# Kernel tuning notes

Hardware: AMD Instinct MI355X
Metric: run time of the kernel (lower is better)

Reference implementation:

```python
import jax, jax.numpy as jnp
import numpy as np

RATIO = 0.25
RADIUS = 0.2
K = 32  # max_num_neighbors


def fps_single(pos, M):
    """Farthest point sampling on one cloud. pos: [N,3] -> idx [M] (start at index 0)."""
    d0 = jnp.sum((pos - pos[0]) ** 2, axis=-1)  # [N] min sq-dist to selected set

    def step(mind, _):
        nxt = jnp.argmax(mind)
        d = jnp.sum((pos - pos[nxt]) ** 2, axis=-1)
        return jnp.minimum(mind, d), nxt

    _, rest = jax.lax.scan(step, d0, None, length=M - 1)
    return jnp.concatenate([jnp.zeros((1,), dtype=rest.dtype), rest])


def mlp(h, W0, b0, W1, b1, W2, b2):
    h = jax.nn.relu(h @ W0 + b0)
    h = jax.nn.relu(h @ W1 + b1)
    h = jax.nn.relu(h @ W2 + b2)
    return h


def setup_inputs() -> dict:
    key = jax.random.key(0)
    ks = jax.random.split(key, 8)
    B, N, C = 8, 8192, 64
    x = jax.random.normal(ks[0], (B, N, C), dtype=jnp.float32)
    pos = jax.random.uniform(ks[1], (B, N, 3), dtype=jnp.float32)
    W0 = jax.random.normal(ks[2], (C + 3, 64), dtype=jnp.float32) * 0.05
    b0 = jnp.zeros((64,), dtype=jnp.float32)
    W1 = jax.random.normal(ks[3], (64, 64), dtype=jnp.float32) * 0.05
    b1 = jnp.zeros((64,), dtype=jnp.float32)
    W2 = jax.random.normal(ks[4], (64, 128), dtype=jnp.float32) * 0.05
    b2 = jnp.zeros((128,), dtype=jnp.float32)
    return {"x": x, "pos": pos, "W0": W0, "b0": b0, "W1": W1, "b1": b1, "W2": W2, "b2": b2}


def reference(x, pos, W0, b0, W1, b1, W2, b2):
    B, N, C = x.shape
    M = int(N * RATIO)
    # 1) FPS per cloud
    idx = jax.vmap(lambda p: fps_single(p, M))(pos)                 # [B, M]
    pos_s = jnp.take_along_axis(pos, idx[..., None], axis=1)        # [B, M, 3]
    # 2) radius ball query: k-nearest (k=K) then mask out > radius.
    #    neighbor selection carries no gradient in the original -> stop_gradient.
    d2 = jax.lax.stop_gradient(
        jnp.sum((pos_s[:, :, None, :] - pos[:, None, :, :]) ** 2, axis=-1))  # [B, M, N]
    negd, nbr = jax.lax.top_k(-d2, K)                               # [B, M, K]
    valid = (-negd) <= RADIUS ** 2                                  # self is always valid (d=0)
    # 3) gather + PointConv message: mlp(concat(x_j, pos_j - pos_i)), max aggr
    x_j = jax.vmap(lambda xb, ib: xb[ib])(x, nbr)                   # [B, M, K, C]
    pos_j = jax.vmap(lambda pb, ib: pb[ib])(pos, nbr)               # [B, M, K, 3]
    feat = jnp.concatenate([x_j, pos_j - pos_s[:, :, None, :]], axis=-1)  # [B, M, K, C+3]
    h = mlp(feat, W0, b0, W1, b1, W2, b2)                           # [B, M, K, 128]
    h = jnp.where(valid[..., None], h, jnp.full_like(h, -1e9))
    x1 = jnp.max(h, axis=2)                                         # [B, M, 128]
    return x1, pos_s
```

## Files before the change

kernel.cpp:

```cpp
#include <hip/hip_runtime.h>
#include <hip/hip_bf16.h>
#include <hip/hip_fp16.h>

#define NB 8
#define NP 8192
#define NC 64
#define NM 2048
#define NK 32
#define RAD2 0.04f

typedef unsigned int u32;
typedef unsigned long long u64;
typedef _Float16 f16x8 __attribute__((ext_vector_type(8)));
typedef float f32x4 __attribute__((ext_vector_type(4)));

__device__ __forceinline__ float d2e(float ax, float ay, float az,
                                     float bx, float by, float bz) {
    float dx = __fsub_rn(ax, bx), dy = __fsub_rn(ay, by), dz = __fsub_rn(az, bz);
    return __fadd_rn(__fadd_rn(__fmul_rn(dx, dx), __fmul_rn(dy, dy)), __fmul_rn(dz, dz));
}

__device__ __forceinline__ int spread3(int v) {
    return (v & 1) | ((v & 2) << 2) | ((v & 4) << 4);
}

#define RED64(CTRL) do {                                                              \
    u32 hi_ = (u32)(k >> 32), lo_ = (u32)k;                                           \
    u32 h2_ = (u32)__builtin_amdgcn_update_dpp((int)hi_, (int)hi_, (CTRL), 0xF, 0xF, false); \
    u32 l2_ = (u32)__builtin_amdgcn_update_dpp((int)lo_, (int)lo_, (CTRL), 0xF, 0xF, false); \
    u64 o_ = ((u64)h2_ << 32) | l2_;                                                  \
    if (o_ > k) k = o_;                                                               \
} while (0)

#define DPPF(V, CTRL) __int_as_float(__builtin_amdgcn_update_dpp(                     \
    __float_as_int(V), __float_as_int(V), (CTRL), 0xF, 0xF, false))

#define WREDMIN(V) do { V = fminf(V, DPPF(V, 0x111)); V = fminf(V, DPPF(V, 0x112));   \
    V = fminf(V, DPPF(V, 0x114)); V = fminf(V, DPPF(V, 0x118));                       \
    V = fminf(V, DPPF(V, 0x142)); V = fminf(V, DPPF(V, 0x143)); } while (0)
#define WREDMAX(V) do { V = fmaxf(V, DPPF(V, 0x111)); V = fmaxf(V, DPPF(V, 0x112));   \
    V = fmaxf(V, DPPF(V, 0x114)); V = fmaxf(V, DPPF(V, 0x118));                       \
    V = fmaxf(V, DPPF(V, 0x142)); V = fmaxf(V, DPPF(V, 0x143)); } while (0)

__device__ __forceinline__ float rl63(float v) {
    return __int_as_float(__builtin_amdgcn_readlane(__float_as_int(v), 63));
}

#define FPT 8
__global__ __launch_bounds__(1024, 1) void fps_kernel(const float* __restrict__ pos,
                                                      float* __restrict__ pos_s) {
    __shared__ float4 sp4[NP];
    __shared__ u32 hist[512], cursor[512];
    __shared__ u64 gkey[3];
    __shared__ u32 pos0srt;

    const int b = blockIdx.x;
    const int tid = threadIdx.x;
    const int lane = tid & 63;
    const float* pb = pos + (size_t)b * (NP * 3);

    float ax[FPT], ay[FPT], az[FPT];
    int key[FPT];
    {
        float f[24];
        const float4* src = (const float4*)(pb + tid * 24);
#pragma unroll
        for (int v = 0; v < 6; ++v) *(float4*)&f[v * 4] = src[v];
#pragma unroll
        for (int j = 0; j < FPT; ++j) {
            ax[j] = f[3 * j]; ay[j] = f[3 * j + 1]; az[j] = f[3 * j + 2];
            int qx = min(7, max(0, (int)(ax[j] * 8.0f)));
            int qy = min(7, max(0, (int)(ay[j] * 8.0f)));
            int qz = min(7, max(0, (int)(az[j] * 8.0f)));
            key[j] = (spread3(qx) << 2) | (spread3(qy) << 1) | spread3(qz);
        }
    }
    if (tid < 512) hist[tid] = 0;
    __syncthreads();
#pragma unroll
    for (int j = 0; j < FPT; ++j) atomicAdd(&hist[key[j]], 1);
    __syncthreads();
    for (int off = 1; off < 512; off <<= 1) {
        u32 v = 0;
        if (tid < 512 && tid >= off) v = hist[tid - off];
        __syncthreads();
        if (tid < 512) hist[tid] += v;
        __syncthreads();
    }
    if (tid < 512) cursor[tid] = (tid == 0) ? 0u : hist[tid - 1];
    if (tid == 0) { gkey[0] = 0; gkey[1] = 0; gkey[2] = 0; }
    __syncthreads();
#pragma unroll
    for (int j = 0; j < FPT; ++j) {
        int dst = (int)atomicAdd(&cursor[key[j]], 1);
        u32 orig = tid * FPT + j;
        sp4[dst] = make_float4(ax[j], ay[j], az[j],
                               __uint_as_float((8191u - orig) << 13));
        if (orig == 0) pos0srt = (u32)dst;
    }
    __syncthreads();

    const int base = tid * FPT;
    const float4 s0 = sp4[pos0srt];
    float px[FPT], py[FPT], pz[FPT];
    u64 mkey[FPT];
    float lox, hix, loy, hiy, loz, hiz;
#pragma unroll
    for (int j = 0; j < FPT; ++j) {
        float4 v = sp4[base + j];
        px[j] = v.x; py[j] = v.y; pz[j] = v.z;
        float d = d2e(v.x, v.y, v.z, s0.x, s0.y, s0.z);
        u32 lo = __float_as_uint(v.w) | (u32)(base + j);
        mkey[j] = ((u64)__float_as_uint(d) << 32) | lo;
        if (j == 0) {
            lox = hix = px[0]; loy = hiy = py[0]; loz = hiz = pz[0];
        } else {
            lox = fminf(lox, px[j]); hix = fmaxf(hix, px[j]);
            loy = fminf(loy, py[j]); hiy = fmaxf(hiy, py[j]);
            loz = fminf(loz, pz[j]); hiz = fmaxf(hiz, pz[j]);
        }
    }
    float wlox, whix, wloy, whiy, wloz, whiz;
    { float v;
      v = lox; WREDMIN(v); wlox = rl63(v);
      v = hix; WREDMAX(v); whix = rl63(v);
      v = loy; WREDMIN(v); wloy = rl63(v);
      v = hiy; WREDMAX(v); whiy = rl63(v);
      v = loz; WREDMIN(v); wloz = rl63(v);
      v = hiz; WREDMAX(v); whiz = rl63(v);
    }
    float* outp = pos_s + (size_t)b * (NM * 3);
    if (tid == 0) { outp[0] = s0.x; outp[1] = s0.y; outp[2] = s0.z; }
    u64 ck = mkey[0];
#pragma unroll
    for (int j = 1; j < FPT; ++j) ck = (mkey[j] > ck) ? mkey[j] : ck;
    u64 wkey;
    { u64 k = ck;
      RED64(0x111); RED64(0x112); RED64(0x114);
      RED64(0x118); RED64(0x142); RED64(0x143);
      wkey = k; }
    float wmindf = __uint_as_float((u32)(wkey >> 32));

    int slot = 1, prv = 0;
    for (int t = 1; t < NM; ++t) {
        if (lane == 63) atomicMax(&gkey[slot], wkey);
        __syncthreads();
        u64 gk = gkey[slot];
        if (tid == 0) gkey[prv] = 0;
        const int srt = (int)(gk & 0x1FFFu);
        const float4 sv = sp4[srt];
        if (tid == 0) { outp[3 * t] = sv.x; outp[3 * t + 1] = sv.y; outp[3 * t + 2] = sv.z; }
        float wgx = fmaxf(fmaxf(__fsub_rn(wlox, sv.x), __fsub_rn(sv.x, whix)), 0.0f);
        float wgy = fmaxf(fmaxf(__fsub_rn(wloy, sv.y), __fsub_rn(sv.y, whiy)), 0.0f);
        float wgz = fmaxf(fmaxf(__fsub_rn(wloz, sv.z), __fsub_rn(sv.z, whiz)), 0.0f);
        float wbnd = wgx * wgx + wgy * wgy + wgz * wgz;
        if (wbnd * 0.999999f < wmindf) {
            float gx = fmaxf(fmaxf(__fsub_rn(lox, sv.x), __fsub_rn(sv.x, hix)), 0.0f);
            float gy = fmaxf(fmaxf(__fsub_rn(loy, sv.y), __fsub_rn(sv.y, hiy)), 0.0f);
            float gz = fmaxf(fmaxf(__fsub_rn(loz, sv.z), __fsub_rn(sv.z, hiz)), 0.0f);
            float bnd = gx * gx + gy * gy + gz * gz;
            float cvf = __uint_as_float((u32)(ck >> 32));
            bool u = (bnd * 0.999999f < cvf);
            if (__ballot(u)) {
                __builtin_amdgcn_s_setprio(1);
                if (u) {
                    u64 nk = 0;
#pragma unroll
                    for (int j = 0; j < FPT; ++j) {
                        float d = d2e(px[j], py[j], pz[j], sv.x, sv.y, sv.z);
                        u32 hi = min((u32)(mkey[j] >> 32), __float_as_uint(d));
                        u64 nm = ((u64)hi << 32) | (u32)mkey[j];
                        mkey[j] = nm;
                        nk = (j == 0) ? nm : ((nm > nk) ? nm : nk);
                    }
                    ck = nk;
                }
                u64 k = ck;
                RED64(0x111); RED64(0x112); RED64(0x114);
                RED64(0x118); RED64(0x142); RED64(0x143);
                wkey = k;
                wmindf = __uint_as_float((u32)(wkey >> 32));
                __builtin_amdgcn_s_setprio(0);
            }
        }
        prv = slot; slot = (slot == 2) ? 0 : slot + 1;
    }
}

#define GQ 8
#define CAP 768
__global__ __launch_bounds__(256, 1) void knn_kernel(const float* __restrict__ pos,
                                                     const float* __restrict__ pos_s,
                                                     int* __restrict__ nbr) {
    __shared__ u64 keys[GQ][CAP];
    __shared__ int cnt[GQ];
    const int qbase = blockIdx.x * GQ;
    const int b = qbase >> 11;
    const int tid = threadIdx.x;
    if (tid < GQ) cnt[tid] = 0;
    for (int i = tid; i < GQ * NK; i += 256) nbr[qbase * NK + i] = -1;

    float qx[GQ], qy[GQ], qz[GQ];
#pragma unroll
    for (int q = 0; q < GQ; ++q) {
        qx[q] = pos_s[(qbase + q) * 3];
        qy[q] = pos_s[(qbase + q) * 3 + 1];
        qz[q] = pos_s[(qbase + q) * 3 + 2];
    }
    __syncthreads();

    const float* pb = pos + (size_t)b * (NP * 3);
    for (int i = 0; i < NP / 256; ++i) {
        int p = tid + (i << 8);
        float x = pb[3 * p], y = pb[3 * p + 1], z = pb[3 * p + 2];
#pragma unroll
        for (int q = 0; q < GQ; ++q) {
            float d = d2e(x, y, z, qx[q], qy[q], qz[q]);
            if (d <= RAD2) {
                int slot = atomicAdd(&cnt[q], 1);
                if (slot < CAP) keys[q][slot] = ((u64)__float_as_uint(d) << 32) | (u32)p;
            }
        }
    }
    __syncthreads();

    for (int q = 0; q < GQ; ++q) {
        int c = min(cnt[q], CAP);
        for (int j = tid; j < c; j += 256) {
            u64 key = keys[q][j];
            int rank = 0;
            for (int t2 = 0; t2 < c; ++t2) rank += (keys[q][t2] < key) ? 1 : 0;
            if (rank < NK) nbr[(qbase + q) * NK + rank] = (int)(u32)(key & 0xFFFFFFFFull);
        }
    }
}

#define FPAD 104
#define HPAD 72
#define TG 8
__global__ __launch_bounds__(512, 1) void mlp_kernel(
    const float* __restrict__ x, const float* __restrict__ pos,
    const float* __restrict__ W0, const float* __restrict__ b0,
    const float* __restrict__ W1, const float* __restrict__ b1,
    const float* __restrict__ W2, const float* __restrict__ b2,
    const float* __restrict__ pos_s, const int* __restrict__ nbr,
    float* __restrict__ x1) {
    __shared__ _Float16 feat[256 * FPAD];
    __shared__ _Float16 h1[256 * HPAD];
    __shared__ _Float16 wt0[64 * FPAD];
    __shared__ _Float16 wt1[64 * HPAD];
    __shared__ _Float16 wt2[128 * HPAD];
    __shared__ float bias0[64], bias1[64], bias2[128];
    __shared__ int vld[256];

    const int tid = threadIdx.x;
    const int g0 = blockIdx.x * TG;
    const int b = g0 >> 11;

    for (int idx = tid; idx < 64 * FPAD; idx += 512) {
        int c2 = idx / FPAD, j = idx - c2 * FPAD;
        wt0[idx] = (_Float16)((j < 67) ? W0[j * 64 + c2] : 0.0f);
    }
    for (int idx = tid; idx < 64 * HPAD; idx += 512) {
        int c2 = idx / HPAD, j = idx - c2 * HPAD;
        wt1[idx] = (_Float16)((j < 64) ? W1[j * 64 + c2] : 0.0f);
    }
    for (int idx = tid; idx < 128 * HPAD; idx += 512) {
        int c2 = idx / HPAD, j = idx - c2 * HPAD;
        wt2[idx] = (_Float16)((j < 64) ? W2[j * 128 + c2] : 0.0f);
    }
    if (tid < 64) { bias0[tid] = b0[tid]; bias1[tid] = b1[tid]; }
    else if (tid < 192) bias2[tid - 64] = b2[tid - 64];

    {
        int r = tid >> 1, half = tid & 1;
        int g = g0 + (r >> 5), k = r & 31;
        int nid = nbr[g * NK + k];
        int nid2 = nid < 0 ? 0 : nid;
        const float* xr = x + ((size_t)b * NP + nid2) * NC + half * 32;
        _Float16* dst = &feat[r * FPAD + half * 32];
#pragma unroll
        for (int i = 0; i < 8; ++i) {
            float4 v = *(const float4*)(xr + i * 4);
            dst[i * 4 + 0] = (_Float16)v.x; dst[i * 4 + 1] = (_Float16)v.y;
            dst[i * 4 + 2] = (_Float16)v.z; dst[i * 4 + 3] = (_Float16)v.w;
        }
        if (half) {
            const float* pj = pos + ((size_t)b * NP + nid2) * 3;
            const float* ps = pos_s + (size_t)g * 3;
            feat[r * FPAD + 64] = (_Float16)(pj[0] - ps[0]);
            feat[r * FPAD + 65] = (_Float16)(pj[1] - ps[1]);
            feat[r * FPAD + 66] = (_Float16)(pj[2] - ps[2]);
#pragma unroll
            for (int j = 67; j < 96; ++j) feat[r * FPAD + j] = (_Float16)0.0f;
        } else {
            vld[r] = (nid >= 0) ? 1 : 0;
        }
    }
    __syncthreads();

    const int lane = tid & 63, w = tid >> 6;
    const int rb = w * 32;
    const int ar = lane & 15;
    const int kg = lane >> 4;

    {
        f32x4 acc[2][4] = {};
#pragma unroll
        for (int kt = 0; kt < 3; ++kt) {
            f16x8 a0 = *(const f16x8*)&feat[(rb + ar) * FPAD + kt * 32 + kg * 8];
            f16x8 a1 = *(const f16x8*)&feat[(rb + 16 + ar) * FPAD + kt * 32 + kg * 8];
#pragma unroll
            for (int nt = 0; nt < 4; ++nt) {
                f16x8 bb = *(const f16x8*)&wt0[(nt * 16 + ar) * FPAD + kt * 32 + kg * 8];
                acc[0][nt] = __builtin_amdgcn_mfma_f32_16x16x32_f16(a0, bb, acc[0][nt], 0, 0, 0);
                acc[1][nt] = __builtin_amdgcn_mfma_f32_16x16x32_f16(a1, bb, acc[1][nt], 0, 0, 0);
            }
        }
#pragma unroll
        for (int mt = 0; mt < 2; ++mt)
#pragma unroll
            for (int nt = 0; nt < 4; ++nt)
#pragma unroll
                for (int ri = 0; ri < 4; ++ri) {
                    int row = rb + mt * 16 + kg * 4 + ri;
                    int col = nt * 16 + ar;
                    float v = fmaxf(acc[mt][nt][ri] + bias0[col], 0.0f);
                    h1[row * HPAD + col] = (_Float16)v;
                }
    }
    __syncthreads();

    _Float16* h2 = feat;
    {
        f32x4 acc[2][4] = {};
#pragma unroll
        for (int kt = 0; kt < 2; ++kt) {
            f16x8 a0 = *(const f16x8*)&h1[(rb + ar) * HPAD + kt * 32 + kg * 8];
            f16x8 a1 = *(const f16x8*)&h1[(rb + 16 + ar) * HPAD + kt * 32 + kg * 8];
#pragma unroll
            for (int nt = 0; nt < 4; ++nt) {
                f16x8 bb = *(const f16x8*)&wt1[(nt * 16 + ar) * HPAD + kt * 32 + kg * 8];
                acc[0][nt] = __builtin_amdgcn_mfma_f32_16x16x32_f16(a0, bb, acc[0][nt], 0, 0, 0);
                acc[1][nt] = __builtin_amdgcn_mfma_f32_16x16x32_f16(a1, bb, acc[1][nt], 0, 0, 0);
            }
        }
#pragma unroll
        for (int mt = 0; mt < 2; ++mt)
#pragma unroll
            for (int nt = 0; nt < 4; ++nt)
#pragma unroll
                for (int ri = 0; ri < 4; ++ri) {
                    int row = rb + mt * 16 + kg * 4 + ri;
                    int col = nt * 16 + ar;
                    float v = fmaxf(acc[mt][nt][ri] + bias1[col], 0.0f);
                    h2[row * HPAD + col] = (_Float16)v;
                }
    }
    __syncthreads();

    {
        f32x4 acc[2][8] = {};
#pragma unroll
        for (int kt = 0; kt < 2; ++kt) {
            f16x8 a0 = *(const f16x8*)&h2[(rb + ar) * HPAD + kt * 32 + kg * 8];
            f16x8 a1 = *(const f16x8*)&h2[(rb + 16 + ar) * HPAD + kt * 32 + kg * 8];
#pragma unroll
            for (int nt = 0; nt < 8; ++nt) {
                f16x8 bb = *(const f16x8*)&wt2[(nt * 16 + ar) * HPAD + kt * 32 + kg * 8];
                acc[0][nt] = __builtin_amdgcn_mfma_f32_16x16x32_f16(a0, bb, acc[0][nt], 0, 0, 0);
                acc[1][nt] = __builtin_amdgcn_mfma_f32_16x16x32_f16(a1, bb, acc[1][nt], 0, 0, 0);
            }
        }
        const int g = g0 + w;
#pragma unroll
        for (int nt = 0; nt < 8; ++nt) {
            int col = nt * 16 + ar;
            float bz = bias2[col];
            float bmax = 0.0f;
#pragma unroll
            for (int mt = 0; mt < 2; ++mt)
#pragma unroll
                for (int ri = 0; ri < 4; ++ri) {
                    int row = rb + mt * 16 + kg * 4 + ri;
                    float v = fmaxf(acc[mt][nt][ri] + bz, 0.0f);
                    bmax = fmaxf(bmax, vld[row] ? v : 0.0f);
                }
            bmax = fmaxf(bmax, __shfl_xor(bmax, 16));
            bmax = fmaxf(bmax, __shfl_xor(bmax, 32));
            if (lane < 16) x1[(size_t)g * 128 + nt * 16 + lane] = bmax;
        }
    }
}

extern "C" void kernel_launch(void* const* d_in, const int* in_sizes, int n_in,
                              void* d_out, int out_size, void* d_ws, size_t ws_size,
                              hipStream_t stream) {
    const float* x   = (const float*)d_in[0];
    const float* pos = (const float*)d_in[1];
    const float* W0  = (const float*)d_in[2];
    const float* b0  = (const float*)d_in[3];
    const float* W1  = (const float*)d_in[4];
    const float* b1  = (const float*)d_in[5];
    const float* W2  = (const float*)d_in[6];
    const float* b2  = (const float*)d_in[7];
    float* x1    = (float*)d_out;
    float* pos_s = x1 + (size_t)NB * NM * 128;
    int* nbr = (int*)d_ws;

    fps_kernel<<<NB, 1024, 0, stream>>>(pos, pos_s);
    knn_kernel<<<(NB * NM) / GQ, 256, 0, stream>>>(pos, pos_s, nbr);
    mlp_kernel<<<(NB * NM) / TG, 512, 0, stream>>>(x, pos, W0, b0, W1, b1, W2, b2,
                                                   pos_s, nbr, x1);
}
```

Measured before the change: 1.682 ms.

## Encode quantized winner position in FPS key to defer LDS lookup off critical path

```diff
diff --git a/kernel.cpp b/kernel.cpp
--- a/kernel.cpp
+++ b/kernel.cpp
@@ -8,6 +8,10 @@
 #define NM 2048
 #define NK 32
 #define RAD2 0.04f
+
+#define EPSX 0.00783f
+#define EPSY 0.00783f
+#define EPSZ 0.00392f
 
 typedef unsigned int u32;
 typedef unsigned long long u64;
@@ -52,7 +56,7 @@
     __shared__ float4 sp4[NP];
     __shared__ u32 hist[512], cursor[512];
     __shared__ u64 gkey[3];
-    __shared__ u32 pos0srt;
+    __shared__ float4 s0sh;
 
     const int b = blockIdx.x;
     const int tid = threadIdx.x;
@@ -60,6 +64,7 @@
     const float* pb = pos + (size_t)b * (NP * 3);
 
     float ax[FPT], ay[FPT], az[FPT];
+    u32 pay[FPT];
     int key[FPT];
     {
         float f[24];
@@ -69,12 +74,15 @@
 #pragma unroll
         for (int j = 0; j < FPT; ++j) {
             ax[j] = f[3 * j]; ay[j] = f[3 * j + 1]; az[j] = f[3 * j + 2];
-            int qx = min(7, max(0, (int)(ax[j] * 8.0f)));
-            int qy = min(7, max(0, (int)(ay[j] * 8.0f)));
-            int qz = min(7, max(0, (int)(az[j] * 8.0f)));
-            key[j] = (spread3(qx) << 2) | (spread3(qy) << 1) | spread3(qz);
-        }
-    }
+            int qx = min(63, max(0, (int)(ax[j] * 64.0f)));
+            int qy = min(63, max(0, (int)(ay[j] * 64.0f)));
+            int qz = min(127, max(0, (int)(az[j] * 128.0f)));
+            u32 orig = (u32)(tid * FPT + j);
+            pay[j] = ((8191u - orig) << 19) | ((u32)qx << 13) | ((u32)qy << 7) | (u32)qz;
+            key[j] = (spread3(qx >> 3) << 2) | (spread3(qy >> 3) << 1) | spread3(qz >> 4);
+        }
+    }
+    if (tid == 0) s0sh = make_float4(ax[0], ay[0], az[0], 0.0f);
     if (tid < 512) hist[tid] = 0;
     __syncthreads();
 #pragma unroll
@@ -88,20 +96,16 @@
         __syncthreads();
     }
     if (tid < 512) cursor[tid] = (tid == 0) ? 0u : hist[tid - 1];
-    if (tid == 0) { gkey[0] = 0; gkey[1] = 0; gkey[2] = 0; }
     __syncthreads();
 #pragma unroll
     for (int j = 0; j < FPT; ++j) {
         int dst = (int)atomicAdd(&cursor[key[j]], 1);
-        u32 orig = tid * FPT + j;
-        sp4[dst] = make_float4(ax[j], ay[j], az[j],
-                               __uint_as_float((8191u - orig) << 13));
-        if (orig == 0) pos0srt = (u32)dst;
+        sp4[dst] = make_float4(ax[j], ay[j], az[j], __uint_as_float(pay[j]));
     }
     __syncthreads();
 
     const int base = tid * FPT;
-    const float4 s0 = sp4[pos0srt];
+    const float4 s0 = s0sh;
     float px[FPT], py[FPT], pz[FPT];
     u64 mkey[FPT];
     float lox, hix, loy, hiy, loz, hiz;
@@ -110,8 +114,7 @@
         float4 v = sp4[base + j];
         px[j] = v.x; py[j] = v.y; pz[j] = v.z;
         float d = d2e(v.x, v.y, v.z, s0.x, s0.y, s0.z);
-        u32 lo = __float_as_uint(v.w) | (u32)(base + j);
-        mkey[j] = ((u64)__float_as_uint(d) << 32) | lo;
+        mkey[j] = ((u64)__float_as_uint(d) << 32) | __float_as_uint(v.w);
         if (j == 0) {
             lox = hix = px[0]; loy = hiy = py[0]; loz = hiz = pz[0];
         } else {
@@ -141,28 +144,41 @@
       wkey = k; }
     float wmindf = __uint_as_float((u32)(wkey >> 32));
 
+    __syncthreads();
+#pragma unroll
+    for (int j = 0; j < FPT; ++j)
+        sp4[tid * FPT + j] = make_float4(ax[j], ay[j], az[j], 0.0f);
+    if (tid == 0) { gkey[0] = 0; gkey[1] = 0; gkey[2] = 0; }
+    __syncthreads();
+
     int slot = 1, prv = 0;
     for (int t = 1; t < NM; ++t) {
         if (lane == 63) atomicMax(&gkey[slot], wkey);
         __syncthreads();
         u64 gk = gkey[slot];
         if (tid == 0) gkey[prv] = 0;
-        const int srt = (int)(gk & 0x1FFFu);
-        const float4 sv = sp4[srt];
-        if (tid == 0) { outp[3 * t] = sv.x; outp[3 * t + 1] = sv.y; outp[3 * t + 2] = sv.z; }
-        float wgx = fmaxf(fmaxf(__fsub_rn(wlox, sv.x), __fsub_rn(sv.x, whix)), 0.0f);
-        float wgy = fmaxf(fmaxf(__fsub_rn(wloy, sv.y), __fsub_rn(sv.y, whiy)), 0.0f);
-        float wgz = fmaxf(fmaxf(__fsub_rn(wloz, sv.z), __fsub_rn(sv.z, whiz)), 0.0f);
+        const u32 glo = (u32)gk;
+        const float sqx = ((float)((glo >> 13) & 63u) + 0.5f) * (1.0f / 64.0f);
+        const float sqy = ((float)((glo >> 7) & 63u) + 0.5f) * (1.0f / 64.0f);
+        const float sqz = ((float)(glo & 127u) + 0.5f) * (1.0f / 128.0f);
+        float wgx = fmaxf(fmaxf(wlox - sqx, sqx - whix) - EPSX, 0.0f);
+        float wgy = fmaxf(fmaxf(wloy - sqy, sqy - whiy) - EPSY, 0.0f);
+        float wgz = fmaxf(fmaxf(wloz - sqz, sqz - whiz) - EPSZ, 0.0f);
         float wbnd = wgx * wgx + wgy * wgy + wgz * wgz;
         if (wbnd * 0.999999f < wmindf) {
-            float gx = fmaxf(fmaxf(__fsub_rn(lox, sv.x), __fsub_rn(sv.x, hix)), 0.0f);
-            float gy = fmaxf(fmaxf(__fsub_rn(loy, sv.y), __fsub_rn(sv.y, hiy)), 0.0f);
-            float gz = fmaxf(fmaxf(__fsub_rn(loz, sv.z), __fsub_rn(sv.z, hiz)), 0.0f);
+            float gx = fmaxf(fmaxf(lox - sqx, sqx - hix) - EPSX, 0.0f);
+            float gy = fmaxf(fmaxf(loy - sqy, sqy - hiy) - EPSY, 0.0f);
+            float gz = fmaxf(fmaxf(loz - sqz, sqz - hiz) - EPSZ, 0.0f);
             float bnd = gx * gx + gy * gy + gz * gz;
             float cvf = __uint_as_float((u32)(ck >> 32));
             bool u = (bnd * 0.999999f < cvf);
             if (__ballot(u)) {
                 __builtin_amdgcn_s_setprio(1);
+                const int sid = 8191 - (int)(glo >> 19);
+                const float4 sv = sp4[sid];
+                if (lane == 63 && wkey == gk) {
+                    outp[3 * t] = sv.x; outp[3 * t + 1] = sv.y; outp[3 * t + 2] = sv.z;
+                }
                 if (u) {
                     u64 nk = 0;
 #pragma unroll
```

Measured after the change: 1.929 ms. 1.15x slower.
